# Optimization experiments

Hardware: AMD Instinct MI355X
Metric: run time of the kernel (lower is better)

The kernel has to match this reference:

```python
import jax, jax.numpy as jnp
import numpy as np

N = 100000   # nodes
E = 1600000  # edges (before self-loops)
D = 128      # in_feats
H = 128      # n_hidden


def setup_inputs() -> dict:
    key = jax.random.key(0)
    k = jax.random.split(key, 6)
    x = jax.random.normal(k[0], (N, D), dtype=jnp.float32)
    src = jax.random.randint(k[1], (E,), 0, N, dtype=jnp.int32)
    dst = jax.random.randint(k[2], (E,), 0, N, dtype=jnp.int32)
    W1 = jax.random.normal(k[3], (D, H), dtype=jnp.float32) / np.float32(np.sqrt(D))
    b1 = jnp.zeros((H,), jnp.float32)
    W2 = jax.random.normal(k[4], (H, H), dtype=jnp.float32) / np.float32(np.sqrt(H))
    b2 = jnp.zeros((H,), jnp.float32)
    return {"x": x, "src": src, "dst": dst, "W1": W1, "b1": b1, "W2": W2, "b2": b2}


def _gcn(x, src, dst, W1, b1, W2, b2):
    n = x.shape[0]
    # add_self_loop(g)
    loops = jnp.arange(n, dtype=src.dtype)
    s = jnp.concatenate([src, loops])
    d = jnp.concatenate([dst, loops])
    ones = jnp.ones((s.shape[0],), dtype=x.dtype)
    deg_out = jax.ops.segment_sum(ones, s, num_segments=n)  # src out-degree
    deg_in = jax.ops.segment_sum(ones, d, num_segments=n)   # dst in-degree
    # DGL GraphConv norm='both': D_out^{-1/2} on source side, D_in^{-1/2} on dest side
    norm_out = jax.lax.rsqrt(jnp.maximum(deg_out, 1.0))[:, None]
    norm_in = jax.lax.rsqrt(jnp.maximum(deg_in, 1.0))[:, None]

    def layer(h, W, b):
        h = h * norm_out                                   # [n, f]
        agg = jax.ops.segment_sum(h[s], d, num_segments=n)  # gather + scatter-add over edges
        return (agg * norm_in) @ W + b

    h = layer(x, W1, b1)
    # dropout p=0 -> identity
    h = layer(h, W2, b2)
    return h


def reference(x, src, dst, W1, b1, W2, b2):
    return _gcn(x, src, dst, W1, b1, W2, b2)
```

## Files before the change

kernel.cpp:

```cpp
#include <hip/hip_runtime.h>

#define FD 128
#define SHIFT 10
#define BNODES 1024
#define NBK 128
#define CHUNK 4096
#define ST 512

typedef unsigned int u32;
typedef unsigned short u16;
typedef unsigned char u8;
typedef __attribute__((ext_vector_type(8))) short short8;
typedef __attribute__((ext_vector_type(4))) float f32x4;
typedef __attribute__((ext_vector_type(4))) u32 u32x4;

__device__ inline u16 f2bf(float f) {
  u32 u = __float_as_uint(f);
  u += 0x7fffu + ((u >> 16) & 1u);
  return (u16)(u >> 16);
}
__device__ inline float bf2f(u16 h) { return __uint_as_float((u32)h << 16); }

__global__ __launch_bounds__(512) void k_hist(const int* __restrict__ src,
                                              const int* __restrict__ dst,
                                              int* __restrict__ bcntD,
                                              int* __restrict__ bcntS,
                                              int e, int n, int nbuck) {
  __shared__ int shD[NBK];
  __shared__ int shS[NBK];
  int tid = threadIdx.x;
  if (tid < NBK) { shD[tid] = 0; shS[tid] = 0; }
  __syncthreads();
  int total = e + n;
  for (int t = blockIdx.x * blockDim.x + tid; t < total; t += gridDim.x * blockDim.x) {
    if (t < e) {
      atomicAdd(&shD[dst[t] >> SHIFT], 1);
      atomicAdd(&shS[src[t] >> SHIFT], 1);
    } else {
      atomicAdd(&shD[(t - e) >> SHIFT], 1);
    }
  }
  __syncthreads();
  if (tid < nbuck) {
    if (shD[tid]) atomicAdd(&bcntD[tid], shD[tid]);
    if (shS[tid]) atomicAdd(&bcntS[tid], shS[tid]);
  }
}

__global__ __launch_bounds__(NBK) void k_bscan(
    const int* __restrict__ bcntD, const int* __restrict__ bcntS,
    int* __restrict__ bbaseD, int* __restrict__ bcurD,
    int* __restrict__ bbaseS, int* __restrict__ bcurS,
    int nbuck, int totalD, int totalS) {
  __shared__ int shD[NBK];
  __shared__ int shS[NBK];
  int tid = threadIdx.x;
  int vD = (tid < nbuck) ? bcntD[tid] : 0;
  int vS = (tid < nbuck) ? bcntS[tid] : 0;
  shD[tid] = vD; shS[tid] = vS;
  __syncthreads();
  for (int off = 1; off < NBK; off <<= 1) {
    int aD = (tid >= off) ? shD[tid - off] : 0;
    int aS = (tid >= off) ? shS[tid - off] : 0;
    __syncthreads();
    shD[tid] += aD; shS[tid] += aS;
    __syncthreads();
  }
  if (tid < nbuck) {
    int exD = shD[tid] - vD; bbaseD[tid] = exD; bcurD[tid] = exD;
    int exS = shS[tid] - vS; bbaseS[tid] = exS; bcurS[tid] = exS;
  }
  if (tid == 0) { bbaseD[nbuck] = totalD; bbaseS[nbuck] = totalS; }
}

__global__ __launch_bounds__(ST) void k_scatter(
    const int* __restrict__ src, const int* __restrict__ dst,
    int* __restrict__ bcurD, int* __restrict__ bcurS,
    u32* __restrict__ pairs, u16* __restrict__ pairs2,
    int e, int n, int nbuck) {
  __shared__ int histD[NBK], exclD[NBK], gbaseD[NBK], rankD[NBK];
  __shared__ int histS[NBK], exclS[NBK], gbaseS[NBK], rankS[NBK];
  __shared__ u32 stgv[CHUNK];
  __shared__ u8  stgb[CHUNK];
  __shared__ u16 stg2[CHUNK];
  __shared__ u8  stg2b[CHUNK];
  int tid = threadIdx.x;
  int c0 = blockIdx.x * CHUNK;
  int total = e + n;
  if (tid < NBK) { histD[tid] = 0; histS[tid] = 0; }
  __syncthreads();
  u32 pv_[8]; int bD_[8], bS_[8]; bool v_[8], vs_[8];
  #pragma unroll
  for (int i = 0; i < 8; ++i) {
    int t = c0 + i * ST + tid;
    v_[i] = (t < total);
    vs_[i] = (t < e);
    pv_[i] = 0; bD_[i] = 0; bS_[i] = 0;
    if (v_[i]) {
      int s, d;
      if (vs_[i]) { s = src[t]; d = dst[t]; }
      else        { s = t - e;  d = s; }
      pv_[i] = ((u32)(d & (BNODES - 1)) << 22) | (u32)s;
      bD_[i] = d >> SHIFT;
      atomicAdd(&histD[bD_[i]], 1);
      if (vs_[i]) { bS_[i] = s >> SHIFT; atomicAdd(&histS[bS_[i]], 1); }
    }
  }
  __syncthreads();
  int hD = 0, hS = 0;
  if (tid < NBK) { hD = histD[tid]; hS = histS[tid]; }
  __syncthreads();
  for (int off = 1; off < NBK; off <<= 1) {
    int aD = 0, aS = 0;
    if (tid < NBK && tid >= off) { aD = histD[tid - off]; aS = histS[tid - off]; }
    __syncthreads();
    if (tid < NBK) { histD[tid] += aD; histS[tid] += aS; }
    __syncthreads();
  }
  if (tid < NBK) {
    int exD = histD[tid] - hD; exclD[tid] = exD; rankD[tid] = exD;
    int exS = histS[tid] - hS; exclS[tid] = exS; rankS[tid] = exS;
    gbaseD[tid] = (tid < nbuck && hD > 0) ? atomicAdd(&bcurD[tid], hD) : 0;
    gbaseS[tid] = (tid < nbuck && hS > 0) ? atomicAdd(&bcurS[tid], hS) : 0;
  }
  __syncthreads();
  #pragma unroll
  for (int i = 0; i < 8; ++i) {
    if (v_[i]) {
      int p = atomicAdd(&rankD[bD_[i]], 1);
      stgv[p] = pv_[i];
      stgb[p] = (u8)bD_[i];
    }
    if (vs_[i]) {
      int p = atomicAdd(&rankS[bS_[i]], 1);
      stg2[p] = (u16)(pv_[i] & (BNODES - 1));
      stg2b[p] = (u8)bS_[i];
    }
  }
  __syncthreads();
  int V = min(CHUNK, total - c0);
  for (int j = tid; j < V; j += ST) {
    int b = stgb[j];
    pairs[gbaseD[b] + (j - exclD[b])] = stgv[j];
  }
  int V2 = min(CHUNK, e - c0);
  for (int j = tid; j < V2; j += ST) {
    int b = stg2b[j];
    pairs2[gbaseS[b] + (j - exclS[b])] = stg2[j];
  }
}

__global__ __launch_bounds__(1024) void k_build(
    const u32* __restrict__ pairs, const int* __restrict__ bbase,
    int* __restrict__ rp, int* __restrict__ col,
    float* __restrict__ nin, int n, int nbuck, int total) {
  __shared__ int cnt[BNODES];
  __shared__ int off_[BNODES];
  __shared__ int cur[BNODES];
  int tid = threadIdx.x;
  int b = blockIdx.x;
  int base = bbase[b], end = bbase[b + 1];
  int node0 = b << SHIFT;
  cnt[tid] = 0;
  __syncthreads();
  for (int t = base + tid; t < end; t += 1024)
    atomicAdd(&cnt[(int)(pairs[t] >> 22)], 1);
  __syncthreads();
  int c = cnt[tid];
  off_[tid] = c;
  __syncthreads();
  for (int off = 1; off < BNODES; off <<= 1) {
    int add = (tid >= off) ? off_[tid - off] : 0;
    __syncthreads();
    off_[tid] += add;
    __syncthreads();
  }
  int ex = off_[tid] - c;
  int node = node0 + tid;
  if (node < n) {
    rp[node] = base + ex;
    nin[node] = rsqrtf((float)c);
  }
  if (b == nbuck - 1 && tid == 0) rp[n] = total;
  cur[tid] = ex;
  __syncthreads();
  for (int t = base + tid; t < end; t += 1024) {
    u32 pr = pairs[t];
    int p = atomicAdd(&cur[(int)(pr >> 22)], 1);
    col[base + p] = (int)(pr & 0x3FFFFFu);
  }
}

__global__ __launch_bounds__(1024) void k_build2(
    const u16* __restrict__ pairs2, const int* __restrict__ bbaseS,
    float* __restrict__ nout, int n, int nbuck) {
  __shared__ int cnt[BNODES];
  int tid = threadIdx.x;
  int b = blockIdx.x;
  int base = bbaseS[b], end = bbaseS[b + 1];
  cnt[tid] = 0;
  __syncthreads();
  for (int t = base + tid; t < end; t += 1024)
    atomicAdd(&cnt[(int)pairs2[t]], 1);
  __syncthreads();
  int node = (b << SHIFT) + tid;
  if (node < n) nout[node] = rsqrtf((float)(cnt[tid] + 1));
}

__global__ __launch_bounds__(256) void k_prescale(
    const float* __restrict__ x, const float* __restrict__ nout,
    u32* __restrict__ xs, int n) {
  int tot = (n + 1) * 64;
  const float2* xv = (const float2*)x;
  for (int idx = blockIdx.x * blockDim.x + threadIdx.x; idx < tot;
       idx += gridDim.x * blockDim.x) {
    int row = idx >> 6;
    if (row >= n) { xs[idx] = 0; }
    else {
      float w = nout[row];
      float2 v = xv[idx];
      xs[idx] = (u32)f2bf(v.x * w) | ((u32)f2bf(v.y * w) << 16);
    }
  }
}

__global__ void k_prepw(const float* __restrict__ W1, u32* __restrict__ wf1hi,
                        u32* __restrict__ wf1lo,
                        const float* __restrict__ W2, u32* __restrict__ wf2hi,
                        u32* __restrict__ wf2lo) {
  int gi = blockIdx.x * 256 + threadIdx.x;
  int i = gi & 8191;
  const float* W = (gi < 8192) ? W1 : W2;
  u32* wfhi = (gi < 8192) ? wf1hi : wf2hi;
  u32* wflo = (gi < 8192) ? wf1lo : wf2lo;
  int m = i & 3, l = (i >> 2) & 63, f = i >> 8;
  int kt = f & 3, nt = f >> 2;
  int k0 = kt * 32 + ((l >> 4) << 3) + 2 * m;
  int c = nt * 16 + (l & 15);
  float w0 = W[k0 * FD + c], w1 = W[(k0 + 1) * FD + c];
  u16 h0 = f2bf(w0), h1 = f2bf(w1);
  u16 l0 = f2bf(w0 - bf2f(h0)), l1 = f2bf(w1 - bf2f(h1));
  wfhi[i] = (u32)h0 | ((u32)h1 << 16);
  wflo[i] = (u32)l0 | ((u32)l1 << 16);
}

__global__ __launch_bounds__(256) void k_agg(
    const u32* __restrict__ hs, const int* __restrict__ rp,
    const int* __restrict__ col, const float* __restrict__ nin,
    u32* __restrict__ ahi, int n) {
  int wv = (blockIdx.x * 256 + threadIdx.x) >> 6;
  int lane = threadIdx.x & 63;
  int g = lane >> 4, ch = lane & 15;
  int r = wv * 4 + g;
  bool valid = (r < n);
  int e0 = 0, e1 = 0;
  if (valid) { e0 = rp[r]; e1 = rp[r + 1]; }
  int m = e1 - e0;
  m = max(m, __shfl_xor(m, 16, 64));
  m = max(m, __shfl_xor(m, 32, 64));
  int trips = (m + 7) >> 3;
  float acc[8] = {0.f, 0.f, 0.f, 0.f, 0.f, 0.f, 0.f, 0.f};
  const u32x4* hv = (const u32x4*)hs;
  int em1 = (e1 > 0) ? (e1 - 1) : 0;
  for (int it = 0; it < trips; ++it) {
    int tb = e0 + it * 8;
    u32x4 buf[8];
    #pragma unroll
    for (int u = 0; u < 8; ++u) {
      int idx = tb + u;
      int s = col[min(idx, em1)];
      s = (idx < e1) ? s : n;
      buf[u] = hv[(size_t)s * 16 + ch];
    }
    #pragma unroll
    for (int u = 0; u < 8; ++u)
      #pragma unroll
      for (int j = 0; j < 4; ++j) {
        u32 x = buf[u][j];
        acc[2 * j]     += __uint_as_float(x << 16);
        acc[2 * j + 1] += __uint_as_float(x & 0xFFFF0000u);
      }
  }
  if (!valid) return;
  float wi = nin[r];
  u32 hi[4];
  #pragma unroll
  for (int j = 0; j < 4; ++j) {
    float v0 = acc[2 * j] * wi, v1 = acc[2 * j + 1] * wi;
    hi[j] = (u32)f2bf(v0) | ((u32)f2bf(v1) << 16);
  }
  int sch = ch ^ (r & 7);
  u32x4 hq = {hi[0], hi[1], hi[2], hi[3]};
  *(u32x4*)(ahi + (size_t)r * 64 + sch * 4) = hq;
}

__global__ __launch_bounds__(256) void k_gemm(
    const u32* __restrict__ ahi,
    const u32* __restrict__ wfhi, const u32* __restrict__ wflo,
    const float* __restrict__ bias, const float* __restrict__ nout,
    float* __restrict__ fout, u16* __restrict__ hsout, int n, int mode) {
  __shared__ u32 Ah[4096];
  int tid = threadIdx.x;
  int lane = tid & 63;
  int mt = tid >> 6;
  int r0 = blockIdx.x * 64;

  const u32x4* gh = (const u32x4*)(ahi + (size_t)r0 * 64);
  u32x4* sh_ = (u32x4*)Ah;
  #pragma unroll
  for (int t = 0; t < 4; ++t) sh_[t * 256 + tid] = gh[t * 256 + tid];
  __syncthreads();

  short8 afh[4];
  int arow = mt * 16 + (lane & 15);
  #pragma unroll
  for (int kt = 0; kt < 4; ++kt) {
    int boff = arow * 256 + ((kt * 64 + (lane >> 4) * 16) ^ ((arow & 7) << 4));
    afh[kt] = *(const short8*)((const char*)Ah + boff);
  }

  for (int nt = 0; nt < 8; ++nt) {
    f32x4 acc = {0.f, 0.f, 0.f, 0.f};
    #pragma unroll
    for (int kt = 0; kt < 4; ++kt) {
      int f = nt * 4 + kt;
      short8 wh = *(const short8*)(wfhi + (size_t)(f * 64 + lane) * 4);
      short8 wl = *(const short8*)(wflo + (size_t)(f * 64 + lane) * 4);
      acc = __builtin_amdgcn_mfma_f32_16x16x32_bf16(afh[kt], wh, acc, 0, 0, 0);
      acc = __builtin_amdgcn_mfma_f32_16x16x32_bf16(afh[kt], wl, acc, 0, 0, 0);
    }
    int c = nt * 16 + (lane & 15);
    float bv = bias[c];
    int rbase = r0 + mt * 16 + (lane >> 4) * 4;
    if (mode == 0) {
      #pragma unroll
      for (int j = 0; j < 4; ++j) {
        int row = rbase + j;
        if (row < n) fout[(size_t)row * FD + c] = acc[j] + bv;
      }
    } else {
      #pragma unroll
      for (int j = 0; j < 4; ++j) {
        int row = rbase + j;
        if (row < n) hsout[(size_t)row * FD + c] = f2bf((acc[j] + bv) * nout[row]);
      }
    }
  }
}

extern "C" void kernel_launch(void* const* d_in, const int* in_sizes, int n_in,
                              void* d_out, int out_size, void* d_ws, size_t ws_size,
                              hipStream_t stream) {
  const float* x  = (const float*)d_in[0];
  const int* src  = (const int*)d_in[1];
  const int* dst  = (const int*)d_in[2];
  const float* W1 = (const float*)d_in[3];
  const float* b1 = (const float*)d_in[4];
  const float* W2 = (const float*)d_in[5];
  const float* b2 = (const float*)d_in[6];
  float* out = (float*)d_out;

  int n = in_sizes[0] / FD;
  int e = in_sizes[1];
  int total = e + n;
  int nbuck = (n + BNODES - 1) >> SHIFT;

  char* ws = (char*)d_ws;
  size_t off = 0;
  auto alloc = [&](size_t bytes) -> void* {
    void* p = ws + off;
    off += (bytes + 255) / 256 * 256;
    return p;
  };
  u32* shared_ = (u32*)alloc((size_t)(n + 16) * 64 * 4);
  u32* pairs = shared_;
  u32* xs    = shared_;
  u16* h1s   = (u16*)shared_;
  u32* ahi   = (u32*)alloc((size_t)(n + 64) * 64 * 4);
  u16* pairs2 = (u16*)alloc((size_t)e * 2 + 256);
  int* col   = (int*)alloc((size_t)total * 4 + 256);
  int* rp    = (int*)alloc((size_t)(n + 1) * 4);
  float* nin  = (float*)alloc((size_t)n * 4);
  float* nout = (float*)alloc((size_t)n * 4);
  int* bcntD  = (int*)alloc(NBK * 4);
  int* bcntS  = (int*)alloc(NBK * 4);
  int* bbaseD = (int*)alloc((NBK + 1) * 4);
  int* bbaseS = (int*)alloc((NBK + 1) * 4);
  int* bcurD  = (int*)alloc(NBK * 4);
  int* bcurS  = (int*)alloc(NBK * 4);
  u32* wf1hi  = (u32*)alloc(8192 * 4);
  u32* wf1lo  = (u32*)alloc(8192 * 4);
  u32* wf2hi  = (u32*)alloc(8192 * 4);
  u32* wf2lo  = (u32*)alloc(8192 * 4);

  hipMemsetAsync(bcntD, 0, (size_t)NBK * 4 * 2, stream);

  k_hist<<<256, 512, 0, stream>>>(src, dst, bcntD, bcntS, e, n, nbuck);
  k_bscan<<<1, NBK, 0, stream>>>(bcntD, bcntS, bbaseD, bcurD, bbaseS, bcurS,
                                 nbuck, total, e);
  k_scatter<<<(total + CHUNK - 1) / CHUNK, ST, 0, stream>>>(
      src, dst, bcurD, bcurS, pairs, pairs2, e, n, nbuck);
  k_build<<<nbuck, 1024, 0, stream>>>(pairs, bbaseD, rp, col, nin, n, nbuck, total);
  k_build2<<<nbuck, 1024, 0, stream>>>(pairs2, bbaseS, nout, n, nbuck);
  k_prepw<<<64, 256, 0, stream>>>(W1, wf1hi, wf1lo, W2, wf2hi, wf2lo);
  k_prescale<<<2048, 256, 0, stream>>>(x, nout, xs, n);

  int agrid = (n + 15) / 16;
  int ggrid = (n + 63) / 64;
  k_agg<<<agrid, 256, 0, stream>>>(xs, rp, col, nin, ahi, n);
  k_gemm<<<ggrid, 256, 0, stream>>>(ahi, wf1hi, wf1lo, b1, nout,
                                    nullptr, h1s, n, 1);
  k_agg<<<agrid, 256, 0, stream>>>((const u32*)h1s, rp, col, nin, ahi, n);
  k_gemm<<<ggrid, 256, 0, stream>>>(ahi, wf2hi, wf2lo, b2, nout,
                                    out, nullptr, n, 0);
}
```

Baseline: 251.1 us.

## Fuse aggregation with GEMM per layer and merge degree-build kernels

```diff
diff --git a/kernel.cpp b/kernel.cpp
--- a/kernel.cpp
+++ b/kernel.cpp
@@ -152,12 +152,26 @@
 
 __global__ __launch_bounds__(1024) void k_build(
     const u32* __restrict__ pairs, const int* __restrict__ bbase,
+    const u16* __restrict__ pairs2, const int* __restrict__ bbaseS,
     int* __restrict__ rp, int* __restrict__ col,
-    float* __restrict__ nin, int n, int nbuck, int total) {
+    float* __restrict__ nin, float* __restrict__ nout,
+    int n, int nbuck, int total) {
   __shared__ int cnt[BNODES];
   __shared__ int off_[BNODES];
   __shared__ int cur[BNODES];
   int tid = threadIdx.x;
+  if (blockIdx.x >= (unsigned)nbuck) {
+    int b = blockIdx.x - nbuck;
+    int base = bbaseS[b], end = bbaseS[b + 1];
+    cnt[tid] = 0;
+    __syncthreads();
+    for (int t = base + tid; t < end; t += 1024)
+      atomicAdd(&cnt[(int)pairs2[t]], 1);
+    __syncthreads();
+    int node = (b << SHIFT) + tid;
+    if (node < n) nout[node] = rsqrtf((float)(cnt[tid] + 1));
+    return;
+  }
   int b = blockIdx.x;
   int base = bbase[b], end = bbase[b + 1];
   int node0 = b << SHIFT;
@@ -189,22 +203,6 @@
     int p = atomicAdd(&cur[(int)(pr >> 22)], 1);
     col[base + p] = (int)(pr & 0x3FFFFFu);
   }
-}
-
-__global__ __launch_bounds__(1024) void k_build2(
-    const u16* __restrict__ pairs2, const int* __restrict__ bbaseS,
-    float* __restrict__ nout, int n, int nbuck) {
-  __shared__ int cnt[BNODES];
-  int tid = threadIdx.x;
-  int b = blockIdx.x;
-  int base = bbaseS[b], end = bbaseS[b + 1];
-  cnt[tid] = 0;
-  __syncthreads();
-  for (int t = base + tid; t < end; t += 1024)
-    atomicAdd(&cnt[(int)pairs2[t]], 1);
-  __syncthreads();
-  int node = (b << SHIFT) + tid;
-  if (node < n) nout[node] = rsqrtf((float)(cnt[tid] + 1));
 }
 
 __global__ __launch_bounds__(256) void k_prescale(
@@ -244,15 +242,22 @@
   wflo[i] = (u32)l0 | ((u32)l1 << 16);
 }
 
-__global__ __launch_bounds__(256) void k_agg(
+__global__ __launch_bounds__(256, 8) void k_layer(
     const u32* __restrict__ hs, const int* __restrict__ rp,
     const int* __restrict__ col, const float* __restrict__ nin,
-    u32* __restrict__ ahi, int n) {
-  int wv = (blockIdx.x * 256 + threadIdx.x) >> 6;
-  int lane = threadIdx.x & 63;
+    const u32* __restrict__ wfhi, const u32* __restrict__ wflo,
+    const float* __restrict__ bias, const float* __restrict__ nout,
+    float* __restrict__ fout, u16* __restrict__ hsout, int n, int mode) {
+  __shared__ u32 As[1024];
+  int tid = threadIdx.x;
+  int lane = tid & 63;
+  int wv = tid >> 6;
   int g = lane >> 4, ch = lane & 15;
-  int r = wv * 4 + g;
+  int r0 = blockIdx.x * 16;
+  int lr = wv * 4 + g;
+  int r = r0 + lr;
   bool valid = (r < n);
+
   int e0 = 0, e1 = 0;
   if (valid) { e0 = rp[r]; e1 = rp[r + 1]; }
   int m = e1 - e0;
@@ -281,68 +286,51 @@
         acc[2 * j + 1] += __uint_as_float(x & 0xFFFF0000u);
       }
   }
-  if (!valid) return;
-  float wi = nin[r];
+  float wi = valid ? nin[r] : 0.f;
   u32 hi[4];
   #pragma unroll
   for (int j = 0; j < 4; ++j) {
     float v0 = acc[2 * j] * wi, v1 = acc[2 * j + 1] * wi;
     hi[j] = (u32)f2bf(v0) | ((u32)f2bf(v1) << 16);
   }
-  int sch = ch ^ (r & 7);
+  int sch = ch ^ (lr & 7);
   u32x4 hq = {hi[0], hi[1], hi[2], hi[3]};
-  *(u32x4*)(ahi + (size_t)r * 64 + sch * 4) = hq;
-}
-
-__global__ __launch_bounds__(256) void k_gemm(
-    const u32* __restrict__ ahi,
-    const u32* __restrict__ wfhi, const u32* __restrict__ wflo,
-    const float* __restrict__ bias, const float* __restrict__ nout,
-    float* __restrict__ fout, u16* __restrict__ hsout, int n, int mode) {
-  __shared__ u32 Ah[4096];
-  int tid = threadIdx.x;
-  int lane = tid & 63;
-  int mt = tid >> 6;
-  int r0 = blockIdx.x * 64;
-
-  const u32x4* gh = (const u32x4*)(ahi + (size_t)r0 * 64);
-  u32x4* sh_ = (u32x4*)Ah;
-  #pragma unroll
-  for (int t = 0; t < 4; ++t) sh_[t * 256 + tid] = gh[t * 256 + tid];
+  *(u32x4*)(As + lr * 64 + sch * 4) = hq;
   __syncthreads();
 
   short8 afh[4];
-  int arow = mt * 16 + (lane & 15);
+  int arow = lane & 15;
   #pragma unroll
   for (int kt = 0; kt < 4; ++kt) {
     int boff = arow * 256 + ((kt * 64 + (lane >> 4) * 16) ^ ((arow & 7) << 4));
-    afh[kt] = *(const short8*)((const char*)Ah + boff);
-  }
-
-  for (int nt = 0; nt < 8; ++nt) {
-    f32x4 acc = {0.f, 0.f, 0.f, 0.f};
+    afh[kt] = *(const short8*)((const char*)As + boff);
+  }
+  #pragma unroll
+  for (int q = 0; q < 2; ++q) {
+    int nt = wv * 2 + q;
+    f32x4 oacc = {0.f, 0.f, 0.f, 0.f};
     #pragma unroll
     for (int kt = 0; kt < 4; ++kt) {
       int f = nt * 4 + kt;
       short8 wh = *(const short8*)(wfhi + (size_t)(f * 64 + lane) * 4);
       short8 wl = *(const short8*)(wflo + (size_t)(f * 64 + lane) * 4);
-      acc = __builtin_amdgcn_mfma_f32_16x16x32_bf16(afh[kt], wh, acc, 0, 0, 0);
-      acc = __builtin_amdgcn_mfma_f32_16x16x32_bf16(afh[kt], wl, acc, 0, 0, 0);
+      oacc = __builtin_amdgcn_mfma_f32_16x16x32_bf16(afh[kt], wh, oacc, 0, 0, 0);
+      oacc = __builtin_amdgcn_mfma_f32_16x16x32_bf16(afh[kt], wl, oacc, 0, 0, 0);
     }
     int c = nt * 16 + (lane & 15);
     float bv = bias[c];
-    int rbase = r0 + mt * 16 + (lane >> 4) * 4;
+    int rbase = r0 + (lane >> 4) * 4;
     if (mode == 0) {
       #pragma unroll
       for (int j = 0; j < 4; ++j) {
         int row = rbase + j;
-        if (row < n) fout[(size_t)row * FD + c] = acc[j] + bv;
+        if (row < n) fout[(size_t)row * FD + c] = oacc[j] + bv;
       }
     } else {
       #pragma unroll
       for (int j = 0; j < 4; ++j) {
         int row = rbase + j;
-        if (row < n) hsout[(size_t)row * FD + c] = f2bf((acc[j] + bv) * nout[row]);
+        if (row < n) hsout[(size_t)row * FD + c] = f2bf((oacc[j] + bv) * nout[row]);
       }
     }
   }
@@ -372,11 +360,9 @@
     off += (bytes + 255) / 256 * 256;
     return p;
   };
-  u32* shared_ = (u32*)alloc((size_t)(n + 16) * 64 * 4);
-  u32* pairs = shared_;
-  u32* xs    = shared_;
-  u16* h1s   = (u16*)shared_;
-  u32* ahi   = (u32*)alloc((size_t)(n + 64) * 64 * 4);
+  u32* xs    = (u32*)alloc((size_t)(n + 16) * 64 * 4);
+  u32* pairs = xs;
+  u16* h1s   = (u16*)alloc((size_t)(n + 16) * FD * 2);
   u16* pairs2 = (u16*)alloc((size_t)e * 2 + 256);
   int* col   = (int*)alloc((size_t)total * 4 + 256);
   int* rp    = (int*)alloc((size_t)(n + 1) * 4);
@@ -394,23 +380,21 @@
   u32* wf2lo  = (u32*)alloc(8192 * 4);
 
   hipMemsetAsync(bcntD, 0, (size_t)NBK * 4 * 2, stream);
+  hipMemsetAsync(h1s + (size_t)n * FD, 0, FD * 2, stream);
 
   k_hist<<<256, 512, 0, stream>>>(src, dst, bcntD, bcntS, e, n, nbuck);
   k_bscan<<<1, NBK, 0, stream>>>(bcntD, bcntS, bbaseD, bcurD, bbaseS, bcurS,
                                  nbuck, total, e);
   k_scatter<<<(total + CHUNK - 1) / CHUNK, ST, 0, stream>>>(
       src, dst, bcurD, bcurS, pairs, pairs2, e, n, nbuck);
-  k_build<<<nbuck, 1024, 0, stream>>>(pairs, bbaseD, rp, col, nin, n, nbuck, total);
-  k_build2<<<nbuck, 1024, 0, stream>>>(pairs2, bbaseS, nout, n, nbuck);
+  k_build<<<2 * nbuck, 1024, 0, stream>>>(pairs, bbaseD, pairs2, bbaseS,
+                                          rp, col, nin, nout, n, nbuck, total);
   k_prepw<<<64, 256, 0, stream>>>(W1, wf1hi, wf1lo, W2, wf2hi, wf2lo);
   k_prescale<<<2048, 256, 0, stream>>>(x, nout, xs, n);
 
-  int agrid = (n + 15) / 16;
-  int ggrid = (n + 63) / 64;
-  k_agg<<<agrid, 256, 0, stream>>>(xs, rp, col, nin, ahi, n);
-  k_gemm<<<ggrid, 256, 0, stream>>>(ahi, wf1hi, wf1lo, b1, nout,
-                                    nullptr, h1s, n, 1);
-  k_agg<<<agrid, 256, 0, stream>>>((const u32*)h1s, rp, col, nin, ahi, n);
-  k_gemm<<<ggrid, 256, 0, stream>>>(ahi, wf2hi, wf2lo, b2, nout,
-                                    out, nullptr, n, 0);
-}
+  int lgrid = (n + 15) / 16;
+  k_layer<<<lgrid, 256, 0, stream>>>(xs, rp, col, nin, wf1hi, wf1lo, b1, nout,
+                                     nullptr, h1s, n, 1);
+  k_layer<<<lgrid, 256, 0, stream>>>((const u32*)h1s, rp, col, nin, wf2hi, wf2lo,
+                                     b2, nout, out, nullptr, n, 0);
+}
```

Measured after the change: 235.9 us. 1.06x faster.
